# Performance work log

Hardware: AMD Instinct MI355X
Metric: run time of the kernel (lower is better)

Reference implementation:

```python
import jax, jax.numpy as jnp
from jax import lax
import numpy as np
import math

# --- static config (matches init_kwargs) ---
B, L, C_IN = 64, 1024, 16
D, H, D_FF = 256, 8, 1024
HS, E_LAYERS, OUT = 256, 2, 1
MA, FACTOR = 25, 3
TOP_K = int(FACTOR * math.log(L))  # 20


def _ln(x, g, b, eps=1e-5):
    m = x.mean(-1, keepdims=True)
    v = ((x - m) ** 2).mean(-1, keepdims=True)
    return (x - m) / jnp.sqrt(v + eps) * g + b


def _series_decomp(x, k):
    # x: [B, L, C]; replicate-pad then moving average (AvgPool1d stride 1)
    pad = (k - 1) // 2
    front = jnp.repeat(x[:, :1, :], pad, axis=1)
    end = jnp.repeat(x[:, -1:, :], pad, axis=1)
    xp = jnp.concatenate([front, x, end], axis=1)  # [B, L+k-1, C]
    cs = jnp.cumsum(xp, axis=1)
    cs = jnp.concatenate([jnp.zeros_like(cs[:, :1]), cs], axis=1)
    mm = (cs[:, k:] - cs[:, :-k]) / k  # [B, L, C]
    return x - mm, mm


def _autocorrelation(q, k, v):
    # q,k,v: [B, L, H, E] -> eval-mode Autoformer AutoCorrelation
    Bq, Lq, Hq, Eq = q.shape
    qf = jnp.fft.rfft(q.transpose(0, 2, 3, 1), axis=-1)  # [B,H,E,F]
    kf = jnp.fft.rfft(k.transpose(0, 2, 3, 1), axis=-1)
    corr = jnp.fft.irfft(qf * jnp.conj(kf), n=Lq, axis=-1)  # [B,H,E,L]
    mean_value = corr.mean(axis=(1, 2))  # [B, L]
    weights, delay = lax.top_k(mean_value, TOP_K)  # [B, K]
    tmp_corr = jax.nn.softmax(weights, axis=-1)
    vals = v.transpose(0, 2, 3, 1)  # [B,H,E,L]
    init = jnp.arange(Lq)

    def step(acc, dw):
        d, w = dw  # d: [B] int, w: [B] float
        idx = (init[None, :] + d[:, None]) % Lq  # circular delayed gather == roll
        pat = jnp.take_along_axis(vals, idx[:, None, None, :], axis=-1)
        return acc + pat * w[:, None, None, None], None

    agg, _ = lax.scan(step, jnp.zeros_like(vals), (delay.T, tmp_corr.T))
    return agg.transpose(0, 3, 1, 2)  # [B, L, H, E]


def _forward(x_enc, conv1_w, conv1_b, conv2_w, conv2_b, cnn_ln_g, cnn_ln_b,
             proj_w, proj_b, proj_ln_g, proj_ln_b,
             Wq, bq, Wk, bk, Wv, bv, Wo, bo, Wff1, Wff2,
             rp1_w, rp1_b, rp_ln_g, rp_ln_b, rp2_w, rp2_b):
    Bb = x_enc.shape[0]
    dn = ('NCH', 'OIH', 'NCH')
    # CNN frontend (dropout = identity in eval)
    h = lax.conv_general_dilated(x_enc.transpose(0, 2, 1), conv1_w, (1,), [(1, 1)],
                                 dimension_numbers=dn) + conv1_b[None, :, None]
    h = jax.nn.relu(h)
    h = lax.conv_general_dilated(h, conv2_w, (1,), [(1, 1)],
                                 dimension_numbers=dn) + conv2_b[None, :, None]
    h = jax.nn.relu(h)
    enc = _ln(h.transpose(0, 2, 1), cnn_ln_g, cnn_ln_b)  # [B, L, D]

    pooled_parts = []
    for i in range(E_LAYERS):
        q = (enc @ Wq[i] + bq[i]).reshape(Bb, L, H, D // H)
        k = (enc @ Wk[i] + bk[i]).reshape(Bb, L, H, D // H)
        v = (enc @ Wv[i] + bv[i]).reshape(Bb, L, H, D // H)
        ac = _autocorrelation(q, k, v).reshape(Bb, L, D)
        new_x = ac @ Wo[i] + bo[i]
        x = enc + new_x
        x, _ = _series_decomp(x, MA)
        y = jax.nn.gelu(jnp.einsum('bld,fd->blf', x, Wff1[i]), approximate=False)
        y = jnp.einsum('blf,df->bld', y, Wff2[i])
        enc, _ = _series_decomp(x + y, MA)
        pooled_parts.append(enc[:, -1, :])

    pooled = jnp.concatenate(pooled_parts, axis=-1)  # [B, e_layers*D]
    input_embed = _ln(jax.nn.relu(x_enc.reshape(Bb, -1) @ proj_w + proj_b),
                      proj_ln_g, proj_ln_b)  # [B, HS]
    final = jnp.concatenate([pooled, input_embed], axis=-1)
    o = jax.nn.relu(final @ rp1_w + rp1_b)
    o = _ln(o, rp_ln_g, rp_ln_b)
    o = o @ rp2_w + rp2_b  # [B, 1]
    return o.squeeze(-1)


def setup_inputs() -> dict:
    key = jax.random.key(0)
    ks = iter(jax.random.split(key, 32))

    def nrm(shape, s=0.02):
        return jax.random.normal(next(ks), shape, jnp.float32) * s

    inp = {
        'x_enc': jax.random.normal(next(ks), (B, L, C_IN), jnp.float32),
        'conv1_w': nrm((D, C_IN, 3), 0.1), 'conv1_b': jnp.zeros((D,), jnp.float32),
        'conv2_w': nrm((D, D, 3), 0.05), 'conv2_b': jnp.zeros((D,), jnp.float32),
        'cnn_ln_g': jnp.ones((D,), jnp.float32), 'cnn_ln_b': jnp.zeros((D,), jnp.float32),
        'proj_w': nrm((L * C_IN, HS)), 'proj_b': jnp.zeros((HS,), jnp.float32),
        'proj_ln_g': jnp.ones((HS,), jnp.float32), 'proj_ln_b': jnp.zeros((HS,), jnp.float32),
        'Wq': nrm((E_LAYERS, D, D)), 'bq': jnp.zeros((E_LAYERS, D), jnp.float32),
        'Wk': nrm((E_LAYERS, D, D)), 'bk': jnp.zeros((E_LAYERS, D), jnp.float32),
        'Wv': nrm((E_LAYERS, D, D)), 'bv': jnp.zeros((E_LAYERS, D), jnp.float32),
        'Wo': nrm((E_LAYERS, D, D)), 'bo': jnp.zeros((E_LAYERS, D), jnp.float32),
        'Wff1': nrm((E_LAYERS, D_FF, D)),
        'Wff2': nrm((E_LAYERS, D, D_FF)),
        'rp1_w': nrm((E_LAYERS * D + HS, HS)), 'rp1_b': jnp.zeros((HS,), jnp.float32),
        'rp_ln_g': jnp.ones((HS,), jnp.float32), 'rp_ln_b': jnp.zeros((HS,), jnp.float32),
        'rp2_w': nrm((HS, OUT)), 'rp2_b': jnp.zeros((OUT,), jnp.float32),
    }
    return inp


def reference(x_enc, conv1_w, conv1_b, conv2_w, conv2_b, cnn_ln_g, cnn_ln_b,
              proj_w, proj_b, proj_ln_g, proj_ln_b,
              Wq, bq, Wk, bk, Wv, bv, Wo, bo, Wff1, Wff2,
              rp1_w, rp1_b, rp_ln_g, rp_ln_b, rp2_w, rp2_b):
    return _forward(x_enc, conv1_w, conv1_b, conv2_w, conv2_b, cnn_ln_g, cnn_ln_b,
                    proj_w, proj_b, proj_ln_g, proj_ln_b,
                    Wq, bq, Wk, bk, Wv, bv, Wo, bo, Wff1, Wff2,
                    rp1_w, rp1_b, rp_ln_g, rp_ln_b, rp2_w, rp2_b)
```

## Files before the change

kernel.cpp:

```cpp
#include <hip/hip_runtime.h>
#include <math.h>

#define FLAG_ACC     1
#define FLAG_RELU    2
#define FLAG_GELU    4
#define FLAG_ABF16   8
#define FLAG_OBF16  16
#define FLAG_RESB16 32

typedef __attribute__((ext_vector_type(8))) short short8;
typedef __attribute__((ext_vector_type(4))) short short4v;
typedef __attribute__((ext_vector_type(4))) float f32x4;

__device__ __forceinline__ short f2bf(float f) {
  unsigned u = __builtin_bit_cast(unsigned, f);
  unsigned r = u + 0x7fffu + ((u >> 16) & 1u);
  return (short)(r >> 16);
}
__device__ __forceinline__ float bf2f(short s) {
  unsigned u = ((unsigned)(unsigned short)s) << 16;
  return __builtin_bit_cast(float, u);
}
__device__ __forceinline__ void load_lds16(const void* g, void* lds) {
  __builtin_amdgcn_global_load_lds(
      (const __attribute__((address_space(1))) void*)g,
      (__attribute__((address_space(3))) void*)lds, 16, 0, 0);
}

__global__ __launch_bounds__(256) void gemm_f32(
    const float* __restrict__ A, const float* __restrict__ B, float* __restrict__ C,
    int M, int N, int K, int a_shift,
    const float* __restrict__ bias, const float* __restrict__ residual, int flags)
{
  __shared__ float As[16][65];
  __shared__ float Bs[16][64];
  const int tid = threadIdx.x;
  const int tx = tid & 15, ty = tid >> 4;
  const int row0 = blockIdx.y * 64;
  const int col0 = blockIdx.x * 64;
  int kbeg = 0, kend = K;
  if ((int)gridDim.z > 1) {
    int kchunk = ((K + (int)gridDim.z - 1) / (int)gridDim.z + 15) & ~15;
    kbeg = (int)blockIdx.z * kchunk;
    kend = min(K, kbeg + kchunk);
  }
  float acc[4][4] = {};
  const int a_m = tid >> 2;
  const int a_k = (tid & 3) << 2;
  const int b_n = (tid & 15) << 2;
  const int b_k = tid >> 4;
  for (int k0 = kbeg; k0 < kend; k0 += 16) {
    int srow = row0 + a_m + a_shift;
    float4 av = make_float4(0.f, 0.f, 0.f, 0.f);
    if (srow >= 0 && srow < M)
      av = *reinterpret_cast<const float4*>(A + (long long)srow * K + (k0 + a_k));
    As[a_k + 0][a_m] = av.x; As[a_k + 1][a_m] = av.y;
    As[a_k + 2][a_m] = av.z; As[a_k + 3][a_m] = av.w;
    float4 bv = make_float4(0.f, 0.f, 0.f, 0.f);
    int brow = k0 + b_k;
    if (brow < K)
      bv = *reinterpret_cast<const float4*>(B + (long long)brow * N + (col0 + b_n));
    Bs[b_k][b_n + 0] = bv.x; Bs[b_k][b_n + 1] = bv.y;
    Bs[b_k][b_n + 2] = bv.z; Bs[b_k][b_n + 3] = bv.w;
    __syncthreads();
#pragma unroll
    for (int kk = 0; kk < 16; kk++) {
      float ar[4], br[4];
#pragma unroll
      for (int i = 0; i < 4; i++) ar[i] = As[kk][ty * 4 + i];
#pragma unroll
      for (int j = 0; j < 4; j++) br[j] = Bs[kk][tx * 4 + j];
#pragma unroll
      for (int i = 0; i < 4; i++)
#pragma unroll
        for (int j = 0; j < 4; j++)
          acc[i][j] += ar[i] * br[j];
    }
    __syncthreads();
  }
  if ((int)gridDim.z > 1) {
#pragma unroll
    for (int i = 0; i < 4; i++) {
      int r = row0 + ty * 4 + i; if (r >= M) continue;
#pragma unroll
      for (int j = 0; j < 4; j++) {
        int c = col0 + tx * 4 + j; if (c >= N) continue;
        atomicAdd(&C[(long long)r * N + c], acc[i][j]);
      }
    }
    return;
  }
#pragma unroll
  for (int i = 0; i < 4; i++) {
    int r = row0 + ty * 4 + i; if (r >= M) continue;
#pragma unroll
    for (int j = 0; j < 4; j++) {
      int c = col0 + tx * 4 + j; if (c >= N) continue;
      float v = acc[i][j];
      if (bias)     v += bias[c];
      if (residual) v += residual[(long long)r * N + c];
      if (flags & FLAG_ACC)  v += C[(long long)r * N + c];
      if (flags & FLAG_RELU) v = fmaxf(v, 0.f);
      if (flags & FLAG_GELU) v = 0.5f * v * (1.f + erff(v * 0.70710678118654752f));
      C[(long long)r * N + c] = v;
    }
  }
}

__global__ __launch_bounds__(256) void gemm_bf16_bt(
    const void* __restrict__ Av, const short* __restrict__ Btb, void* __restrict__ Cv,
    const float* __restrict__ residual, const float* __restrict__ bias,
    int M, int N, int K, int lda, int flags, int tapped)
{
  __shared__ __align__(16) short Asl[8192];
  __shared__ __align__(16) short Bsl[8192];
  const int tid = threadIdx.x;
  const int row0 = blockIdx.x * 128;
  const int col0 = blockIdx.y * 128;
  const int lane = tid & 63;
  const int wave = tid >> 6;
  const int wm = (wave >> 1) * 64;
  const int wn = (wave & 1) * 64;
  const int fm = lane & 15;
  const int k8c = lane >> 4;
  const int mr = tid >> 1;
  const int mkc = (tid & 1) * 4;
  const int msw = mr & 7;
  const bool a_dma = (flags & FLAG_ABF16) && !tapped;

  f32x4 acc[4][4] = {};
  for (int k0 = 0; k0 < K; k0 += 64) {
    __syncthreads();
#pragma unroll
    for (int u = 0; u < 4; u++) {
      int p = (wave * 4 + u) * 64 + lane;
      int r = p >> 3;
      int kc = (p & 7) ^ (r & 7);
      load_lds16(Btb + (long long)(col0 + r) * K + k0 + kc * 8,
                 (char*)Bsl + (wave * 4 + u) * 1024);
    }
    if (a_dma) {
      const short* Ab = (const short*)Av;
#pragma unroll
      for (int u = 0; u < 4; u++) {
        int p = (wave * 4 + u) * 64 + lane;
        int r = p >> 3;
        int kc = (p & 7) ^ (r & 7);
        load_lds16(Ab + (long long)(row0 + r) * lda + k0 + kc * 8,
                   (char*)Asl + (wave * 4 + u) * 1024);
      }
    } else {
      int arow = row0 + mr + (tapped ? (k0 >> 8) - 1 : 0);
      int acol = tapped ? (k0 & 255) : k0;
      bool ok = (arow >= 0 && arow < M);
      if (flags & FLAG_ABF16) {
        const short* ga = (const short*)Av + (long long)arow * lda + acol + mkc * 8;
        short8 z;
#pragma unroll
        for (int u = 0; u < 8; u++) z[u] = 0;
#pragma unroll
        for (int j = 0; j < 4; j++) {
          short8 v = ok ? *(const short8*)(ga + j * 8) : z;
          *(short8*)&Asl[(mr * 8 + ((mkc + j) ^ msw)) * 8] = v;
        }
      } else {
        const float* ga = (const float*)Av + (long long)arow * lda + acol + mkc * 8;
#pragma unroll
        for (int j = 0; j < 4; j++) {
          float4 f0 = make_float4(0.f,0.f,0.f,0.f), f1 = f0;
          if (ok) { f0 = *(const float4*)(ga + j * 8); f1 = *(const float4*)(ga + j * 8 + 4); }
          short8 v;
          v[0]=f2bf(f0.x); v[1]=f2bf(f0.y); v[2]=f2bf(f0.z); v[3]=f2bf(f0.w);
          v[4]=f2bf(f1.x); v[5]=f2bf(f1.y); v[6]=f2bf(f1.z); v[7]=f2bf(f1.w);
          *(short8*)&Asl[(mr * 8 + ((mkc + j) ^ msw)) * 8] = v;
        }
      }
    }
    __syncthreads();
#pragma unroll
    for (int kk8 = 0; kk8 < 8; kk8 += 4) {
      short8 af[4], bf[4];
#pragma unroll
      for (int i = 0; i < 4; i++) {
        int r = wm + i * 16 + fm;
        af[i] = *(short8*)&Asl[(r * 8 + ((kk8 + k8c) ^ (r & 7))) * 8];
      }
#pragma unroll
      for (int j = 0; j < 4; j++) {
        int r = wn + j * 16 + fm;
        bf[j] = *(short8*)&Bsl[(r * 8 + ((kk8 + k8c) ^ (r & 7))) * 8];
      }
#pragma unroll
      for (int i = 0; i < 4; i++)
#pragma unroll
        for (int j = 0; j < 4; j++)
          acc[i][j] = __builtin_amdgcn_mfma_f32_16x16x32_bf16(af[i], bf[j], acc[i][j], 0, 0, 0);
    }
  }
#pragma unroll
  for (int i = 0; i < 4; i++) {
    const int mbase = row0 + wm + i * 16 + (lane >> 4) * 4;
#pragma unroll
    for (int j = 0; j < 4; j++) {
      const int n = col0 + wn + j * 16 + fm;
      const float bs = bias ? bias[n] : 0.f;
#pragma unroll
      for (int r = 0; r < 4; r++) {
        long long idx = (long long)(mbase + r) * N + n;
        float v = acc[i][j][r] + bs;
        if (residual) {
          if (flags & FLAG_RESB16) v += bf2f(((const short*)residual)[idx]);
          else                     v += residual[idx];
        }
        if (flags & FLAG_ACC)  v += ((const float*)Cv)[idx];
        if (flags & FLAG_RELU) v = fmaxf(v, 0.f);
        if (flags & FLAG_GELU) v = 0.5f * v * (1.f + erff(v * 0.70710678118654752f));
        if (flags & FLAG_OBF16) ((short*)Cv)[idx] = f2bf(v);
        else                    ((float*)Cv)[idx] = v;
      }
    }
  }
}

__global__ __launch_bounds__(256) void gemm_qkT(
    const short* __restrict__ Ab, const short* __restrict__ Bth,
    const short* __restrict__ Btl, float* __restrict__ QT,
    const float* __restrict__ bias, int K)
{
  __shared__ __align__(16) char smem[24576];
  short* Asl = (short*)smem;
  short* Bhi = (short*)(smem + 8192);
  short* Blo = (short*)(smem + 16384);
  const int tid = threadIdx.x;
  const int row0 = blockIdx.x * 128;
  const int col0 = blockIdx.y * 128;
  const int lane = tid & 63;
  const int wave = tid >> 6;
  const int wm = (wave >> 1) * 64;
  const int wn = (wave & 1) * 64;
  const int fm = lane & 15;
  const int k8c = lane >> 4;

  f32x4 acc[4][4] = {};
  for (int k0 = 0; k0 < K; k0 += 32) {
    __syncthreads();
#pragma unroll
    for (int u = 0; u < 2; u++) {
      int p = (wave + u * 4) * 64 + lane;
      int r = p >> 2;
      int kc = (p & 3) ^ ((r >> 1) & 3);
      long long ao = (long long)(row0 + r) * 256 + k0 + kc * 8;
      long long go = (long long)(col0 + r) * K + k0 + kc * 8;
      int lo = (wave + u * 4) * 1024;
      load_lds16(Ab + ao, (char*)Asl + lo);
      load_lds16(Bth + go, (char*)Bhi + lo);
      load_lds16(Btl + go, (char*)Blo + lo);
    }
    __syncthreads();
    short8 af[4], bh[4], bl[4];
#pragma unroll
    for (int i = 0; i < 4; i++) {
      int r = wm + i * 16 + fm;
      af[i] = *(short8*)&Asl[(r * 4 + (k8c ^ ((r >> 1) & 3))) * 8];
    }
#pragma unroll
    for (int j = 0; j < 4; j++) {
      int r = wn + j * 16 + fm;
      int p = (r * 4 + (k8c ^ ((r >> 1) & 3))) * 8;
      bh[j] = *(short8*)&Bhi[p];
      bl[j] = *(short8*)&Blo[p];
    }
#pragma unroll
    for (int i = 0; i < 4; i++)
#pragma unroll
      for (int j = 0; j < 4; j++) {
        acc[i][j] = __builtin_amdgcn_mfma_f32_16x16x32_bf16(af[i], bh[j], acc[i][j], 0, 0, 0);
        acc[i][j] = __builtin_amdgcn_mfma_f32_16x16x32_bf16(af[i], bl[j], acc[i][j], 0, 0, 0);
      }
  }
#pragma unroll
  for (int i = 0; i < 4; i++) {
    const int mbase = row0 + wm + i * 16 + (lane >> 4) * 4;
    const int bb = mbase >> 10;
    const int l  = mbase & 1023;
#pragma unroll
    for (int j = 0; j < 4; j++) {
      const int n = col0 + wn + j * 16 + fm;
      const float bs = bias[n];
      float4 o = make_float4(acc[i][j][0] + bs, acc[i][j][1] + bs,
                             acc[i][j][2] + bs, acc[i][j][3] + bs);
      *(float4*)&QT[((long long)(bb * 512 + n) << 10) + l] = o;
    }
  }
}

#define SKW(i) ((i) + ((i) >> 5))

__device__ __forceinline__ int rev4_10(int f) {
  return ((f & 3) << 8) | (((f >> 2) & 3) << 6) | (((f >> 4) & 3) << 4)
       | (((f >> 6) & 3) << 2) | ((f >> 8) & 3);
}

template<int M, bool INV, int NCH>
__device__ __forceinline__ void fft_stageN(float2 (*__restrict__ buf)[1056],
                                           const float2* __restrict__ tw, int t) {
  constexpr int LOG2M = (M == 256) ? 8 : (M == 64) ? 6 : (M == 16) ? 4 : (M == 4) ? 2 : 0;
  const int j = t & (M - 1);
  const int base = ((t >> LOG2M) << (LOG2M + 2)) | j;
  float2 w = tw[SKW(j << (8 - LOG2M))];
  const float c1 = w.x, s1 = INV ? -w.y : w.y;
  const float c2 = c1 * c1 - s1 * s1, s2 = 2.f * c1 * s1;
  const float c3 = c2 * c1 - s2 * s1, s3 = c2 * s1 + s2 * c1;
#pragma unroll
  for (int ch = 0; ch < NCH; ch++) {
    float2* s = buf[ch];
    float2 a0 = s[SKW(base)];
    float2 b0 = s[SKW(base + M)];
    float2 d0 = s[SKW(base + 2 * M)];
    float2 e0 = s[SKW(base + 3 * M)];
    float t0r = a0.x + d0.x, t0i = a0.y + d0.y;
    float t1r = a0.x - d0.x, t1i = a0.y - d0.y;
    float t2r = b0.x + e0.x, t2i = b0.y + e0.y;
    float t3r = b0.x - e0.x, t3i = b0.y - e0.y;
    float y0r = t0r + t2r, y0i = t0i + t2i;
    float y2r = t0r - t2r, y2i = t0i - t2i;
    float y1r, y1i, y3r, y3i;
    if (!INV) { y1r = t1r + t3i; y1i = t1i - t3r; y3r = t1r - t3i; y3i = t1i + t3r; }
    else      { y1r = t1r - t3i; y1i = t1i + t3r; y3r = t1r + t3i; y3i = t1i - t3r; }
    s[SKW(base)]         = make_float2(y0r, y0i);
    s[SKW(base + M)]     = make_float2(y1r * c1 - y1i * s1, y1r * s1 + y1i * c1);
    s[SKW(base + 2 * M)] = make_float2(y2r * c2 - y2i * s2, y2r * s2 + y2i * c2);
    s[SKW(base + 3 * M)] = make_float2(y3r * c3 - y3i * s3, y3r * s3 + y3i * c3);
  }
}

__global__ __launch_bounds__(256) void fft_cross(
    const float* __restrict__ QT, float* __restrict__ Rpart)
{
  __shared__ float2 buf[4][1056];
  __shared__ float2 tw[264];
  const int tid = threadIdx.x;
  const int b = blockIdx.x & 63;
  const int g = blockIdx.x >> 6;
  {
    float s, c;
    sincosf(-1.5707963267948966f * (float)tid * (1.f / 256.f), &s, &c);
    tw[SKW(tid)] = make_float2(c, s);
  }
  const float* Qb = QT + (long long)b * 524288;
  const int c0 = g * 16;
  float4 qv[4], kv[4];
#pragma unroll
  for (int c = 0; c < 4; c++) {
    qv[c] = *(const float4*)(Qb + ((long long)(c0 + c) << 10) + tid * 4);
    kv[c] = *(const float4*)(Qb + ((long long)(256 + c0 + c) << 10) + tid * 4);
  }
  float aR[4] = {0.f, 0.f, 0.f, 0.f}, aI[4] = {0.f, 0.f, 0.f, 0.f};
  __syncthreads();
  for (int q4 = 0; q4 < 4; q4++) {
    const int i0 = tid * 4;
#pragma unroll
    for (int c = 0; c < 4; c++) {
      buf[c][SKW(i0 + 0)] = make_float2(qv[c].x, kv[c].x);
      buf[c][SKW(i0 + 1)] = make_float2(qv[c].y, kv[c].y);
      buf[c][SKW(i0 + 2)] = make_float2(qv[c].z, kv[c].z);
      buf[c][SKW(i0 + 3)] = make_float2(qv[c].w, kv[c].w);
    }
    if (q4 < 3) {
      const int cb = c0 + (q4 + 1) * 4;
#pragma unroll
      for (int c = 0; c < 4; c++) {
        qv[c] = *(const float4*)(Qb + ((long long)(cb + c) << 10) + tid * 4);
        kv[c] = *(const float4*)(Qb + ((long long)(256 + cb + c) << 10) + tid * 4);
      }
    }
    __syncthreads();
    fft_stageN<256, false, 4>(buf, tw, tid); __syncthreads();
    fft_stageN<64,  false, 4>(buf, tw, tid); __syncthreads();
    fft_stageN<16,  false, 4>(buf, tw, tid); __syncthreads();
    fft_stageN<4,   false, 4>(buf, tw, tid); __syncthreads();
    fft_stageN<1,   false, 4>(buf, tw, tid); __syncthreads();
#pragma unroll
    for (int u = 0; u < 4; u++) {
      const int f = tid + (u << 8);
      const int p1 = SKW(rev4_10(f));
      const int p2 = SKW(rev4_10((1024 - f) & 1023));
#pragma unroll
      for (int c = 0; c < 4; c++) {
        float2 z1 = buf[c][p1];
        float2 z2 = buf[c][p2];
        float Qr = 0.5f * (z1.x + z2.x), Qi = 0.5f * (z1.y - z2.y);
        float Kr = 0.5f * (z1.y + z2.y), Ki = 0.5f * (z2.x - z1.x);
        aR[u] += Qr * Kr + Qi * Ki;
        aI[u] += Qi * Kr - Qr * Ki;
      }
    }
    __syncthreads();
  }
  float* Rp = Rpart + (long long)(g * 64 + b) * 2048;
#pragma unroll
  for (int u = 0; u < 4; u++) {
    Rp[tid + (u << 8)] = aR[u];
    Rp[1024 + tid + (u << 8)] = aI[u];
  }
}

__global__ __launch_bounds__(256) void fft_inv(
    const float* __restrict__ Rpart, float* __restrict__ MV)
{
  __shared__ float2 ping[1056], tw[264];
  const int tid = threadIdx.x;
  const int b = blockIdx.x;
  {
    float s, c;
    sincosf(-1.5707963267948966f * (float)tid * (1.f / 256.f), &s, &c);
    tw[SKW(tid)] = make_float2(c, s);
  }
#pragma unroll
  for (int u = 0; u < 4; u++) {
    int f = tid + (u << 8);
    float sr = 0.f, si = 0.f;
#pragma unroll
    for (int g = 0; g < 16; g++) {
      const float* Rp = Rpart + (long long)(g * 64 + b) * 2048;
      sr += Rp[f];
      si += Rp[1024 + f];
    }
    ping[SKW(f)] = make_float2(sr, si);
  }
  __syncthreads();
  float2 (*bp)[1056] = reinterpret_cast<float2 (*)[1056]>(ping);
  fft_stageN<256, true, 1>(bp, tw, tid); __syncthreads();
  fft_stageN<64,  true, 1>(bp, tw, tid); __syncthreads();
  fft_stageN<16,  true, 1>(bp, tw, tid); __syncthreads();
  fft_stageN<4,   true, 1>(bp, tw, tid); __syncthreads();
  fft_stageN<1,   true, 1>(bp, tw, tid); __syncthreads();
  const float sc = 1.f / (1024.f * 256.f);
#pragma unroll
  for (int u = 0; u < 4; u++) {
    int p = tid + (u << 8);
    MV[(long long)b * 1024 + rev4_10(p)] = ping[SKW(p)].x * sc;
  }
}

__global__ void prep_weights(
    const float* __restrict__ conv2_w, const float* __restrict__ Wq,
    const float* __restrict__ Wk, const float* __restrict__ Wff1,
    const float* __restrict__ Wff2,
    const float* __restrict__ bq, const float* __restrict__ bk,
    short* __restrict__ CB2Tb, short* __restrict__ QKTH, short* __restrict__ QKTL,
    short* __restrict__ WFF1b, short* __restrict__ WFF2b, float* __restrict__ BQK)
{
  const int total = 196608 + 262144 + 524288 + 524288 + 1024;
  for (int idx = blockIdx.x * 256 + threadIdx.x; idx < total;
       idx += gridDim.x * 256) {
    int t = idx;
    if (t < 196608) {
      int o = t / 768, rem = t % 768, kk = rem >> 8, i = rem & 255;
      CB2Tb[t] = f2bf(conv2_w[(o * 256 + i) * 3 + kk]);
    } else if ((t -= 196608) < 262144) {
      int L = t >> 17, rem = t & 131071, r = rem >> 8, k = rem & 255;
      float val = (r < 256) ? Wq[L * 65536 + k * 256 + r]
                            : Wk[L * 65536 + k * 256 + (r - 256)];
      short h = f2bf(val);
      QKTH[t] = h;
      QKTL[t] = f2bf(val - bf2f(h));
    } else if ((t -= 262144) < 524288) {
      WFF1b[t] = f2bf(Wff1[t]);
    } else if ((t -= 524288) < 524288) {
      WFF2b[t] = f2bf(Wff2[t]);
    } else {
      t -= 524288;
      int L = t >> 9, j = t & 511;
      BQK[t] = (j < 256) ? bq[L * 256 + j] : bk[L * 256 + (j - 256)];
    }
  }
}

__global__ void vo_finish(const float* __restrict__ WVO, const float* __restrict__ Wo,
                          const float* __restrict__ bv, const float* __restrict__ bo,
                          short* __restrict__ WVOTb, float* __restrict__ BVO)
{
  const int total = 131072 + 512;
  for (int idx = blockIdx.x * 256 + threadIdx.x; idx < total;
       idx += gridDim.x * 256) {
    if (idx < 131072) {
      int L = idx >> 16, rem = idx & 65535, n = rem >> 8, k = rem & 255;
      WVOTb[idx] = f2bf(WVO[L * 65536 + k * 256 + n]);
    } else {
      int j = idx - 131072;
      int L = j >> 8, n = j & 255;
      float acc = bo[L * 256 + n];
      for (int k = 0; k < 256; k++)
        acc += bv[L * 256 + k] * Wo[(long long)L * 65536 + k * 256 + n];
      BVO[j] = acc;
    }
  }
}

__global__ __launch_bounds__(256) void conv1_direct(
    const float* __restrict__ x, const float* __restrict__ w,
    const float* __restrict__ bias, short* __restrict__ out)
{
  __shared__ float xs[66][16];
  const int b = blockIdx.y, lg = blockIdx.x, tid = threadIdx.x;
  const int l0 = lg * 64;
  for (int idx = tid; idx < 1056; idx += 256) {
    int r = idx >> 4, c = idx & 15;
    int l = l0 + r - 1;
    xs[r][c] = (l >= 0 && l < 1024) ? x[((long long)b * 1024 + l) * 16 + c] : 0.f;
  }
  float wr[48];
#pragma unroll
  for (int u = 0; u < 48; u++) wr[u] = w[tid * 48 + u];
  const float bs = bias[tid];
  __syncthreads();
  for (int r = 0; r < 64; r++) {
    float acc = bs;
#pragma unroll
    for (int i = 0; i < 16; i++) {
      acc += xs[r + 0][i] * wr[i * 3 + 0];
      acc += xs[r + 1][i] * wr[i * 3 + 1];
      acc += xs[r + 2][i] * wr[i * 3 + 2];
    }
    out[((long long)b * 1024 + l0 + r) * 256 + tid] = f2bf(fmaxf(acc, 0.f));
  }
}

__global__ void fixup_conv_b(short* __restrict__ h, const short* __restrict__ src,
                             const float* __restrict__ w, const float* __restrict__ bias)
{
  int b = blockIdx.x >> 1;
  int l = (blockIdx.x & 1) ? 1023 : 0;
  int o = threadIdx.x;
  float acc = bias[o];
  for (int kk = 0; kk < 3; kk++) {
    int t = l + kk - 1;
    if (t < 0 || t > 1023) continue;
    const short* srow = src + ((long long)b * 1024 + t) * 256;
    const float* wrow = w + (long long)o * 256 * 3 + kk;
    for (int i = 0; i < 256; i++) acc += bf2f(srow[i]) * wrow[(long long)i * 3];
  }
  h[((long long)b * 1024 + l) * 256 + o] = f2bf(fmaxf(acc, 0.f));
}

__global__ __launch_bounds__(256) void ln_rows4(
    const float* __restrict__ in, float* __restrict__ out,
    const float* __restrict__ g, const float* __restrict__ b,
    int prerelu, int out_stride, int out_off)
{
  const int row = blockIdx.x * 4 + (threadIdx.x >> 6);
  const int lane = threadIdx.x & 63;
  float4 x = ((const float4*)(in + (long long)row * 256))[lane];
  if (prerelu) {
    x.x = fmaxf(x.x, 0.f); x.y = fmaxf(x.y, 0.f);
    x.z = fmaxf(x.z, 0.f); x.w = fmaxf(x.w, 0.f);
  }
  float s = x.x + x.y + x.z + x.w;
#pragma unroll
  for (int o = 32; o > 0; o >>= 1) s += __shfl_xor(s, o, 64);
  float mean = s * (1.f / 256.f);
  float4 d = make_float4(x.x - mean, x.y - mean, x.z - mean, x.w - mean);
  float s2 = d.x * d.x + d.y * d.y + d.z * d.z + d.w * d.w;
#pragma unroll
  for (int o = 32; o > 0; o >>= 1) s2 += __shfl_xor(s2, o, 64);
  float rsd = rsqrtf(s2 * (1.f / 256.f) + 1e-5f);
  float4 gg = ((const float4*)g)[lane];
  float4 bb = ((const float4*)b)[lane];
  float4 o4 = make_float4(d.x * rsd * gg.x + bb.x, d.y * rsd * gg.y + bb.y,
                          d.z * rsd * gg.z + bb.z, d.w * rsd * gg.w + bb.w);
  ((float4*)(out + (long long)row * out_stride + out_off))[lane] = o4;
}

__global__ __launch_bounds__(256) void ln_rows4bb(
    const short* __restrict__ in, short* __restrict__ out,
    const float* __restrict__ g, const float* __restrict__ b)
{
  const int row = blockIdx.x * 4 + (threadIdx.x >> 6);
  const int lane = threadIdx.x & 63;
  short4v xb = ((const short4v*)in)[(long long)row * 64 + lane];
  float4 x = make_float4(bf2f(xb[0]), bf2f(xb[1]), bf2f(xb[2]), bf2f(xb[3]));
  float s = x.x + x.y + x.z + x.w;
#pragma unroll
  for (int o = 32; o > 0; o >>= 1) s += __shfl_xor(s, o, 64);
  float mean = s * (1.f / 256.f);
  float4 d = make_float4(x.x - mean, x.y - mean, x.z - mean, x.w - mean);
  float s2 = d.x * d.x + d.y * d.y + d.z * d.z + d.w * d.w;
#pragma unroll
  for (int o = 32; o > 0; o >>= 1) s2 += __shfl_xor(s2, o, 64);
  float rsd = rsqrtf(s2 * (1.f / 256.f) + 1e-5f);
  float4 gg = ((const float4*)g)[lane];
  float4 bb = ((const float4*)b)[lane];
  short4v o4;
  o4[0] = f2bf(d.x * rsd * gg.x + bb.x);
  o4[1] = f2bf(d.y * rsd * gg.y + bb.y);
  o4[2] = f2bf(d.z * rsd * gg.z + bb.z);
  o4[3] = f2bf(d.w * rsd * gg.w + bb.w);
  ((short4v*)out)[(long long)row * 64 + lane] = o4;
}

__global__ void decomp4bf(const short* __restrict__ in, short* __restrict__ out,
                          float* __restrict__ fin, int finoff)
{
  const int id = blockIdx.x;
  const int c = id & 7;
  const int s = id >> 3;
  const int b = c + 8 * (s >> 8);
  const int lg = s & 255;
  const int l = lg * 4 + (threadIdx.x >> 6);
  const int c4 = threadIdx.x & 63;
  const short4v* base = (const short4v*)(in + (long long)b * 262144);
  float4 acc = make_float4(0.f, 0.f, 0.f, 0.f);
#pragma unroll
  for (int j = -12; j <= 12; j++) {
    int t = l + j;
    t = t < 0 ? 0 : (t > 1023 ? 1023 : t);
    short4v x = base[t * 64 + c4];
    acc.x += bf2f(x[0]); acc.y += bf2f(x[1]);
    acc.z += bf2f(x[2]); acc.w += bf2f(x[3]);
  }
  short4v x0 = base[l * 64 + c4];
  float4 o = make_float4(bf2f(x0[0]) - acc.x * (1.f / 25.f),
                         bf2f(x0[1]) - acc.y * (1.f / 25.f),
                         bf2f(x0[2]) - acc.z * (1.f / 25.f),
                         bf2f(x0[3]) - acc.w * (1.f / 25.f));
  short4v ob;
  ob[0] = f2bf(o.x); ob[1] = f2bf(o.y); ob[2] = f2bf(o.z); ob[3] = f2bf(o.w);
  ((short4v*)out)[((long long)b * 1024 + l) * 64 + c4] = ob;
  if (l == 1023) {
    float* f = fin + (long long)b * 768 + finoff + c4 * 4;
    f[0] = o.x; f[1] = o.y; f[2] = o.z; f[3] = o.w;
  }
}

__global__ void decomp4b(const short* __restrict__ in, short* __restrict__ out)
{
  const int id = blockIdx.x;
  const int c = id & 7;
  const int s = id >> 3;
  const int b = c + 8 * (s >> 8);
  const int lg = s & 255;
  const int l = lg * 4 + (threadIdx.x >> 6);
  const int c4 = threadIdx.x & 63;
  const short4v* base = (const short4v*)(in + (long long)b * 262144);
  float4 acc = make_float4(0.f, 0.f, 0.f, 0.f);
#pragma unroll
  for (int j = -12; j <= 12; j++) {
    int t = l + j;
    t = t < 0 ? 0 : (t > 1023 ? 1023 : t);
    short4v x = base[t * 64 + c4];
    acc.x += bf2f(x[0]); acc.y += bf2f(x[1]);
    acc.z += bf2f(x[2]); acc.w += bf2f(x[3]);
  }
  short4v x0 = base[l * 64 + c4];
  short4v o;
  o[0] = f2bf(bf2f(x0[0]) - acc.x * (1.f / 25.f));
  o[1] = f2bf(bf2f(x0[1]) - acc.y * (1.f / 25.f));
  o[2] = f2bf(bf2f(x0[2]) - acc.z * (1.f / 25.f));
  o[3] = f2bf(bf2f(x0[3]) - acc.w * (1.f / 25.f));
  ((short4v*)(out + (long long)b * 262144))[l * 64 + c4] = o;
}

__global__ __launch_bounds__(64) void topk_softmax_wave(
    const float* __restrict__ mv, float* __restrict__ wts, int* __restrict__ dly)
{
  const int b = blockIdx.x, lane = threadIdx.x;
  float v[16];
#pragma unroll
  for (int j = 0; j < 16; j++)
    v[j] = mv[(long long)b * 1024 + lane + 64 * j];
  float selv = 0.f; int seli = 0;
  for (int it = 0; it < 20; it++) {
    float bv = -1e30f; int bi = 0x7fffffff;
#pragma unroll
    for (int j = 0; j < 16; j++) {
      float x = v[j]; int idx = lane + 64 * j;
      if (x > bv || (x == bv && idx < bi)) { bv = x; bi = idx; }
    }
#pragma unroll
    for (int off = 32; off > 0; off >>= 1) {
      float ov = __shfl_xor(bv, off, 64);
      int   oi = __shfl_xor(bi, off, 64);
      if (ov > bv || (ov == bv && oi < bi)) { bv = ov; bi = oi; }
    }
    if (lane == it) { selv = bv; seli = bi; }
    if ((bi & 63) == lane) v[bi >> 6] = -1e30f;
  }
  const float w0 = __shfl(selv, 0, 64);
  float e = (lane < 20) ? __expf(selv - w0) : 0.f;
  float s = e;
#pragma unroll
  for (int off = 32; off > 0; off >>= 1) s += __shfl_xor(s, off, 64);
  if (lane < 20) {
    wts[b * 20 + lane] = e / s;
    dly[b * 20 + lane] = seli;
  }
}

__global__ void agg4b(const short* __restrict__ enc, const float* __restrict__ wts,
                      const int* __restrict__ dly, short* __restrict__ out)
{
  const int id = blockIdx.x;
  const int c = id & 7;
  const int s = id >> 3;
  const int b = c + 8 * (s >> 8);
  const int lg = s & 255;
  const int l = lg * 4 + (threadIdx.x >> 6);
  const int c4 = threadIdx.x & 63;
  const short4v* vb = (const short4v*)(enc + (long long)b * 262144);
  float4 acc = make_float4(0.f, 0.f, 0.f, 0.f);
  for (int kk = 0; kk < 20; kk++) {
    int d = dly[b * 20 + kk];
    float w = wts[b * 20 + kk];
    short4v x = vb[((l + d) & 1023) * 64 + c4];
    acc.x += w * bf2f(x[0]); acc.y += w * bf2f(x[1]);
    acc.z += w * bf2f(x[2]); acc.w += w * bf2f(x[3]);
  }
  short4v o;
  o[0] = f2bf(acc.x); o[1] = f2bf(acc.y); o[2] = f2bf(acc.z); o[3] = f2bf(acc.w);
  ((short4v*)(out + (long long)b * 262144))[l * 64 + c4] = o;
}

__global__ void init_bias(float* __restrict__ C, const float* __restrict__ bias)
{
  C[(long long)blockIdx.x * 256 + threadIdx.x] = bias[threadIdx.x];
}

__global__ void rp2_kernel(const float* __restrict__ x, const float* __restrict__ w,
                           const float* __restrict__ bias, float* __restrict__ out)
{
  __shared__ float red[4];
  int b = blockIdx.x, tid = threadIdx.x;
  float p = x[b * 256 + tid] * w[tid];
#pragma unroll
  for (int o = 32; o > 0; o >>= 1) p += __shfl_down(p, o, 64);
  if ((tid & 63) == 0) red[tid >> 6] = p;
  __syncthreads();
  if (tid == 0) out[b] = red[0] + red[1] + red[2] + red[3] + bias[0];
}

static inline void gemm(hipStream_t s, const float* A, const float* B, float* C,
                        int M, int N, int K, int shift, const float* bias,
                        const float* res, int flags, int splitz = 1)
{
  dim3 g((N + 63) / 64, (M + 63) / 64, splitz);
  gemm_f32<<<g, dim3(256), 0, s>>>(A, B, C, M, N, K, shift, bias, res, flags);
}

extern "C" void kernel_launch(void* const* d_in, const int* in_sizes, int n_in,
                              void* d_out, int out_size, void* d_ws, size_t ws_size,
                              hipStream_t stream)
{
  const float* x_enc  = (const float*)d_in[0];
  const float* conv1_w= (const float*)d_in[1];
  const float* conv1_b= (const float*)d_in[2];
  const float* conv2_w= (const float*)d_in[3];
  const float* conv2_b= (const float*)d_in[4];
  const float* cnn_g  = (const float*)d_in[5];
  const float* cnn_b  = (const float*)d_in[6];
  const float* proj_w = (const float*)d_in[7];
  const float* proj_b = (const float*)d_in[8];
  const float* pln_g  = (const float*)d_in[9];
  const float* pln_b  = (const float*)d_in[10];
  const float* Wq     = (const float*)d_in[11];
  const float* bq     = (const float*)d_in[12];
  const float* Wk     = (const float*)d_in[13];
  const float* bk     = (const float*)d_in[14];
  const float* Wv     = (const float*)d_in[15];
  const float* bv     = (const float*)d_in[16];
  const float* Wo     = (const float*)d_in[17];
  const float* bo     = (const float*)d_in[18];
  const float* Wff1   = (const float*)d_in[19];
  const float* Wff2   = (const float*)d_in[20];
  const float* rp1_w  = (const float*)d_in[21];
  const float* rp1_b  = (const float*)d_in[22];
  const float* rln_g  = (const float*)d_in[23];
  const float* rln_b  = (const float*)d_in[24];
  const float* rp2_w  = (const float*)d_in[25];
  const float* rp2_b  = (const float*)d_in[26];
  (void)in_sizes; (void)n_in;

  const size_t BLD = 64ull * 1024 * 256;
  size_t need;
  {
    size_t o = 3 * BLD
             + 98304 + 131072 + 131072 + 262144 + 262144
             + 65536 + 512 + 1024
             + 1048576 + 1280 + 1280 + 16384 + 49152 + 16384 + 16384;
    need = o * sizeof(float);
  }
  if (ws_size < need) {
    hipMemsetAsync(d_out, 0, (size_t)out_size * sizeof(float), stream);
    return;
  }

  float* ws = (float*)d_ws;
  size_t off = 0;
  auto alloc = [&](size_t n) { float* p = ws + off; off += n; return p; };
  float* BUF0 = alloc(BLD);
  float* BUF1 = alloc(BLD);
  float* BUF2 = alloc(BLD);
  short* CB2Tb = (short*)alloc(98304);
  short* QKTH  = (short*)alloc(131072);
  short* QKTL  = (short*)alloc(131072);
  short* WFF1b = (short*)alloc(262144);
  short* WFF2b = (short*)alloc(262144);
  short* WVOTb = (short*)alloc(65536);
  float* BVO  = alloc(512);
  float* BQK  = alloc(1024);
  float* MV16 = alloc(1048576);
  float* WTS  = alloc(1280);
  int*   DLY  = (int*)alloc(1280);
  float* PE   = alloc(16384);
  float* FIN  = alloc(49152);
  float* O1   = alloc(16384);
  float* O2   = alloc(16384);
  float* WVO  = BUF0;
  short* ENC  = (short*)BUF2;
  float* QT   = BUF0;
  float* RP   = BUF2 + 8388608;
  float* MV   = MV16;

  const int M = 65536;
  dim3 blk(256);

  prep_weights<<<1024, blk, 0, stream>>>(conv2_w, Wq, Wk, Wff1, Wff2, bq, bk,
                                         CB2Tb, QKTH, QKTL, WFF1b, WFF2b, BQK);
  for (int i = 0; i < 2; i++)
    gemm(stream, Wv + (size_t)i * 65536, Wo + (size_t)i * 65536,
         WVO + (size_t)i * 65536, 256, 256, 256, 0, nullptr, nullptr, 0);
  vo_finish<<<516, blk, 0, stream>>>(WVO, Wo, bv, bo, WVOTb, BVO);

  conv1_direct<<<dim3(16, 64), blk, 0, stream>>>(x_enc, conv1_w, conv1_b, (short*)BUF0);
  gemm_bf16_bt<<<dim3(512, 2), blk, 0, stream>>>(
      BUF0, CB2Tb, BUF1, nullptr, conv2_b, M, 256, 768, 256,
      FLAG_ABF16 | FLAG_RELU | FLAG_OBF16, 1);
  fixup_conv_b<<<128, blk, 0, stream>>>((short*)BUF1, (const short*)BUF0,
                                        conv2_w, conv2_b);
  ln_rows4bb<<<16384, blk, 0, stream>>>((const short*)BUF1, ENC, cnn_g, cnn_b);

  for (int i = 0; i < 2; i++) {
    gemm_qkT<<<dim3(512, 4), blk, 0, stream>>>(
        ENC, QKTH + (size_t)i * 131072, QKTL + (size_t)i * 131072,
        QT, BQK + i * 512, 256);
    fft_cross<<<dim3(1024), blk, 0, stream>>>(QT, RP);
    fft_inv<<<64, blk, 0, stream>>>(RP, MV);
    topk_softmax_wave<<<64, dim3(64), 0, stream>>>(MV, WTS, DLY);
    agg4b<<<dim3(16384), blk, 0, stream>>>(ENC, WTS, DLY, (short*)BUF0);
    gemm_bf16_bt<<<dim3(512, 2), blk, 0, stream>>>(
        BUF0, WVOTb + (size_t)i * 65536, BUF1, (const float*)ENC, BVO + i * 256,
        M, 256, 256, 256, FLAG_ABF16 | FLAG_OBF16 | FLAG_RESB16, 0);
    decomp4b<<<16384, blk, 0, stream>>>((const short*)BUF1, (short*)BUF0);
    for (int c = 0; c < 2; c++) {
      const short* xd = (const short*)BUF0 + (size_t)c * 32768 * 256;
      gemm_bf16_bt<<<dim3(256, 8), blk, 0, stream>>>(
          xd, WFF1b + (size_t)i * 262144, BUF2, nullptr, nullptr,
          32768, 1024, 256, 256, FLAG_ABF16 | FLAG_GELU | FLAG_OBF16, 0);
      gemm_bf16_bt<<<dim3(256, 2), blk, 0, stream>>>(
          BUF2, WFF2b + (size_t)i * 262144,
          (short*)BUF1 + (size_t)c * 32768 * 256,
          (const float*)xd, nullptr,
          32768, 256, 1024, 1024, FLAG_ABF16 | FLAG_RESB16 | FLAG_OBF16, 0);
    }
    decomp4bf<<<16384, blk, 0, stream>>>((const short*)BUF1, ENC, FIN, i * 256);
  }

  init_bias<<<64, blk, 0, stream>>>(PE, proj_b);
  gemm(stream, x_enc, proj_w, PE, 64, 256, 16384, 0, nullptr, nullptr, 0, 32);
  ln_rows4<<<16, blk, 0, stream>>>(PE, FIN, pln_g, pln_b, 1, 768, 512);
  init_bias<<<64, blk, 0, stream>>>(O1, rp1_b);
  gemm(stream, FIN, rp1_w, O1, 64, 256, 768, 0, nullptr, nullptr, 0, 4);
  ln_rows4<<<16, blk, 0, stream>>>(O1, O2, rln_g, rln_b, 1, 256, 0);
  rp2_kernel<<<64, blk, 0, stream>>>(O2, rp2_w, rp2_b, (float*)d_out);
}
```

Measured before the change: 1.493 ms.

## Double-buffer LDS tiles in bf16 GEMM kernels to overlap loads with MFMA

```diff
diff --git a/kernel.cpp b/kernel.cpp
--- a/kernel.cpp
+++ b/kernel.cpp
@@ -112,8 +112,8 @@
     const float* __restrict__ residual, const float* __restrict__ bias,
     int M, int N, int K, int lda, int flags, int tapped)
 {
-  __shared__ __align__(16) short Asl[8192];
-  __shared__ __align__(16) short Bsl[8192];
+  __shared__ __align__(16) short Asl[2][8192];
+  __shared__ __align__(16) short Bsl[2][8192];
   const int tid = threadIdx.x;
   const int row0 = blockIdx.x * 128;
   const int col0 = blockIdx.y * 128;
@@ -128,67 +128,74 @@
   const int msw = mr & 7;
   const bool a_dma = (flags & FLAG_ABF16) && !tapped;
 
-  f32x4 acc[4][4] = {};
-  for (int k0 = 0; k0 < K; k0 += 64) {
-    __syncthreads();
+  short8 sv[4];
+
+  auto stage_dma = [&](int buf, int k0) {
 #pragma unroll
     for (int u = 0; u < 4; u++) {
       int p = (wave * 4 + u) * 64 + lane;
       int r = p >> 3;
       int kc = (p & 7) ^ (r & 7);
       load_lds16(Btb + (long long)(col0 + r) * K + k0 + kc * 8,
-                 (char*)Bsl + (wave * 4 + u) * 1024);
-    }
-    if (a_dma) {
-      const short* Ab = (const short*)Av;
-#pragma unroll
-      for (int u = 0; u < 4; u++) {
-        int p = (wave * 4 + u) * 64 + lane;
-        int r = p >> 3;
-        int kc = (p & 7) ^ (r & 7);
-        load_lds16(Ab + (long long)(row0 + r) * lda + k0 + kc * 8,
-                   (char*)Asl + (wave * 4 + u) * 1024);
+                 (char*)Bsl[buf] + (wave * 4 + u) * 1024);
+      if (a_dma)
+        load_lds16((const short*)Av + (long long)(row0 + r) * lda + k0 + kc * 8,
+                   (char*)Asl[buf] + (wave * 4 + u) * 1024);
+    }
+  };
+  auto loadA = [&](int k0) {
+    int arow = row0 + mr + (tapped ? (k0 >> 8) - 1 : 0);
+    int acol = tapped ? (k0 & 255) : k0;
+    bool ok = (arow >= 0 && arow < M);
+    if (flags & FLAG_ABF16) {
+      const short* ga = (const short*)Av + (long long)arow * lda + acol + mkc * 8;
+      short8 z;
+#pragma unroll
+      for (int u = 0; u < 8; u++) z[u] = 0;
+#pragma unroll
+      for (int j = 0; j < 4; j++) sv[j] = ok ? *(const short8*)(ga + j * 8) : z;
+    } else {
+      const float* ga = (const float*)Av + (long long)arow * lda + acol + mkc * 8;
+#pragma unroll
+      for (int j = 0; j < 4; j++) {
+        float4 f0 = make_float4(0.f,0.f,0.f,0.f), f1 = f0;
+        if (ok) { f0 = *(const float4*)(ga + j * 8); f1 = *(const float4*)(ga + j * 8 + 4); }
+        short8 v;
+        v[0]=f2bf(f0.x); v[1]=f2bf(f0.y); v[2]=f2bf(f0.z); v[3]=f2bf(f0.w);
+        v[4]=f2bf(f1.x); v[5]=f2bf(f1.y); v[6]=f2bf(f1.z); v[7]=f2bf(f1.w);
+        sv[j] = v;
       }
-    } else {
-      int arow = row0 + mr + (tapped ? (k0 >> 8) - 1 : 0);
-      int acol = tapped ? (k0 & 255) : k0;
-      bool ok = (arow >= 0 && arow < M);
-      if (flags & FLAG_ABF16) {
-        const short* ga = (const short*)Av + (long long)arow * lda + acol + mkc * 8;
-        short8 z;
-#pragma unroll
-        for (int u = 0; u < 8; u++) z[u] = 0;
-#pragma unroll
-        for (int j = 0; j < 4; j++) {
-          short8 v = ok ? *(const short8*)(ga + j * 8) : z;
-          *(short8*)&Asl[(mr * 8 + ((mkc + j) ^ msw)) * 8] = v;
-        }
-      } else {
-        const float* ga = (const float*)Av + (long long)arow * lda + acol + mkc * 8;
-#pragma unroll
-        for (int j = 0; j < 4; j++) {
-          float4 f0 = make_float4(0.f,0.f,0.f,0.f), f1 = f0;
-          if (ok) { f0 = *(const float4*)(ga + j * 8); f1 = *(const float4*)(ga + j * 8 + 4); }
-          short8 v;
-          v[0]=f2bf(f0.x); v[1]=f2bf(f0.y); v[2]=f2bf(f0.z); v[3]=f2bf(f0.w);
-          v[4]=f2bf(f1.x); v[5]=f2bf(f1.y); v[6]=f2bf(f1.z); v[7]=f2bf(f1.w);
-          *(short8*)&Asl[(mr * 8 + ((mkc + j) ^ msw)) * 8] = v;
-        }
-      }
-    }
-    __syncthreads();
+    }
+  };
+  auto writeA = [&](int buf) {
+#pragma unroll
+    for (int j = 0; j < 4; j++)
+      *(short8*)&Asl[buf][(mr * 8 + ((mkc + j) ^ msw)) * 8] = sv[j];
+  };
+
+  f32x4 acc[4][4] = {};
+  const int nt = K >> 6;
+  stage_dma(0, 0);
+  if (!a_dma) { loadA(0); writeA(0); }
+  __syncthreads();
+  int cur = 0;
+  for (int t = 0; t < nt; t++) {
+    if (t + 1 < nt) {
+      stage_dma(cur ^ 1, (t + 1) << 6);
+      if (!a_dma) loadA((t + 1) << 6);
+    }
 #pragma unroll
     for (int kk8 = 0; kk8 < 8; kk8 += 4) {
       short8 af[4], bf[4];
 #pragma unroll
       for (int i = 0; i < 4; i++) {
         int r = wm + i * 16 + fm;
-        af[i] = *(short8*)&Asl[(r * 8 + ((kk8 + k8c) ^ (r & 7))) * 8];
+        af[i] = *(short8*)&Asl[cur][(r * 8 + ((kk8 + k8c) ^ (r & 7))) * 8];
       }
 #pragma unroll
       for (int j = 0; j < 4; j++) {
         int r = wn + j * 16 + fm;
-        bf[j] = *(short8*)&Bsl[(r * 8 + ((kk8 + k8c) ^ (r & 7))) * 8];
+        bf[j] = *(short8*)&Bsl[cur][(r * 8 + ((kk8 + k8c) ^ (r & 7))) * 8];
       }
 #pragma unroll
       for (int i = 0; i < 4; i++)
@@ -196,6 +203,9 @@
         for (int j = 0; j < 4; j++)
           acc[i][j] = __builtin_amdgcn_mfma_f32_16x16x32_bf16(af[i], bf[j], acc[i][j], 0, 0, 0);
     }
+    if (!a_dma && t + 1 < nt) writeA(cur ^ 1);
+    __syncthreads();
+    cur ^= 1;
   }
 #pragma unroll
   for (int i = 0; i < 4; i++) {
@@ -227,10 +237,9 @@
     const short* __restrict__ Btl, float* __restrict__ QT,
     const float* __restrict__ bias, int K)
 {
-  __shared__ __align__(16) char smem[24576];
-  short* Asl = (short*)smem;
-  short* Bhi = (short*)(smem + 8192);
-  short* Blo = (short*)(smem + 16384);
+  __shared__ __align__(16) short Asl[2][4096];
+  __shared__ __align__(16) short Bhi[2][4096];
+  __shared__ __align__(16) short Blo[2][4096];
   const int tid = threadIdx.x;
   const int row0 = blockIdx.x * 128;
   const int col0 = blockIdx.y * 128;
@@ -241,9 +250,7 @@
   const int fm = lane & 15;
   const int k8c = lane >> 4;
 
-  f32x4 acc[4][4] = {};
-  for (int k0 = 0; k0 < K; k0 += 32) {
-    __syncthreads();
+  auto stage = [&](int buf, int k0) {
 #pragma unroll
     for (int u = 0; u < 2; u++) {
       int p = (wave + u * 4) * 64 + lane;
@@ -252,23 +259,31 @@
       long long ao = (long long)(row0 + r) * 256 + k0 + kc * 8;
       long long go = (long long)(col0 + r) * K + k0 + kc * 8;
       int lo = (wave + u * 4) * 1024;
-      load_lds16(Ab + ao, (char*)Asl + lo);
-      load_lds16(Bth + go, (char*)Bhi + lo);
-      load_lds16(Btl + go, (char*)Blo + lo);
-    }
-    __syncthreads();
+      load_lds16(Ab + ao, (char*)Asl[buf] + lo);
+      load_lds16(Bth + go, (char*)Bhi[buf] + lo);
+      load_lds16(Btl + go, (char*)Blo[buf] + lo);
+    }
+  };
+
+  f32x4 acc[4][4] = {};
+  const int nt = K >> 5;
+  stage(0, 0);
+  __syncthreads();
+  int cur = 0;
+  for (int t = 0; t < nt; t++) {
+    if (t + 1 < nt) stage(cur ^ 1, (t + 1) << 5);
     short8 af[4], bh[4], bl[4];
 #pragma unroll
     for (int i = 0; i < 4; i++) {
       int r = wm + i * 16 + fm;
-      af[i] = *(short8*)&Asl[(r * 4 + (k8c ^ ((r >> 1) & 3))) * 8];
+      af[i] = *(short8*)&Asl[cur][(r * 4 + (k8c ^ ((r >> 1) & 3))) * 8];
     }
 #pragma unroll
     for (int j = 0; j < 4; j++) {
       int r = wn + j * 16 + fm;
       int p = (r * 4 + (k8c ^ ((r >> 1) & 3))) * 8;
-      bh[j] = *(short8*)&Bhi[p];
-      bl[j] = *(short8*)&Blo[p];
+      bh[j] = *(short8*)&Bhi[cur][p];
+      bl[j] = *(short8*)&Blo[cur][p];
     }
 #pragma unroll
     for (int i = 0; i < 4; i++)
@@ -277,6 +292,8 @@
         acc[i][j] = __builtin_amdgcn_mfma_f32_16x16x32_bf16(af[i], bh[j], acc[i][j], 0, 0, 0);
         acc[i][j] = __builtin_amdgcn_mfma_f32_16x16x32_bf16(af[i], bl[j], acc[i][j], 0, 0, 0);
       }
+    __syncthreads();
+    cur ^= 1;
   }
 #pragma unroll
   for (int i = 0; i < 4; i++) {
```

Result: slower. 1.523 ms (+2.0%).
